# Kernel tuning notes

Measured on AMD Instinct MI355X. Metric: run time of the kernel, lower is better.

The kernel has to match this reference:

```python
import jax, jax.numpy as jnp
import numpy as np

N = 50000   # nodes
E = 800000  # directed edges (self-loops added inside reference)
F_IN, H, C = 128, 96, 32


def setup_inputs() -> dict:
    key = jax.random.key(0)
    ks = jax.random.split(key, 8)
    x = jax.random.normal(ks[0], (N, F_IN), dtype=jnp.float32)
    edge_index = jax.random.randint(ks[1], (2, E), 0, N, dtype=jnp.int64)
    W1 = jax.random.normal(ks[2], (F_IN, H), dtype=jnp.float32) * 0.05
    b1 = jnp.zeros((H,), dtype=jnp.float32)
    W2 = jax.random.normal(ks[3], (H, H), dtype=jnp.float32) * 0.05
    b2 = jnp.zeros((H,), dtype=jnp.float32)
    W3 = jax.random.normal(ks[4], (H, C), dtype=jnp.float32) * 0.05
    b3 = jnp.zeros((C,), dtype=jnp.float32)
    return {"x": x, "edge_index": edge_index, "W1": W1, "b1": b1,
            "W2": W2, "b2": b2, "W3": W3, "b3": b3}


def gcn_conv(x, W, b, src, dst, n):
    """PyG GCNConv: x' = D^{-1/2} (A+I) D^{-1/2} (x W) + b (self-loops in src/dst)."""
    xw = x @ W                                        # [n, out]
    ones = jnp.ones(src.shape[0], dtype=xw.dtype)
    deg = jax.ops.segment_sum(ones, dst, num_segments=n)
    dinv = jnp.where(deg > 0, jax.lax.rsqrt(jnp.maximum(deg, 1.0)), 0.0)
    norm = dinv[src] * dinv[dst]                      # [E+n]
    msg = norm[:, None] * xw[src]                     # gather + scale
    out = jax.ops.segment_sum(msg, dst, num_segments=n)  # scatter-add
    return out + b


def reference(x, edge_index, W1, b1, W2, b2, W3, b3):
    loop = jnp.arange(N, dtype=edge_index.dtype)
    src = jnp.concatenate([edge_index[0], loop])      # add self-loops once
    dst = jnp.concatenate([edge_index[1], loop])
    h = jax.nn.relu(gcn_conv(x, W1, b1, src, dst, N))   # dropout is identity (eval)
    h = jax.nn.relu(gcn_conv(h, W2, b2, src, dst, N))
    h = gcn_conv(h, W3, b3, src, dst, N)
    return jax.nn.log_softmax(h, axis=1)
```

## Files before the change

kernel.cpp:

```cpp
#include <hip/hip_runtime.h>
#include <hip/hip_fp16.h>


typedef _Float16 half8 __attribute__((ext_vector_type(8)));
typedef float f32x4 __attribute__((ext_vector_type(4)));

constexpr int CAP = 64;
constexpr int NPB = 128;
constexpr int NBINS_P = 512;
constexpr int EPB = 4096;
constexpr int BCAP = 2560;

__device__ inline unsigned char f_to_fp8(float f) {
    f = fminf(fmaxf(f, -448.0f), 448.0f);
    unsigned short u = __half_as_ushort(__float2half(f * 0.00390625f));
    unsigned short mag = (unsigned short)((u & 0x7FFF) + 0x40);
    return (unsigned char)(((u >> 8) & 0x80) | (mag >> 7));
}

__device__ inline float2 fp8x2_to_f2_scaled(unsigned int w) {
    unsigned int lo = ((w << 7) & 0x3F80u) | ((w << 8) & 0x8000u);
    unsigned int hi = ((w >> 1) & 0x3F80u) | (w & 0x8000u);
    union { unsigned int u; __half2 h; } cv;
    cv.u = lo | (hi << 16);
    return __half22float2(cv.h);
}

__global__ __launch_bounds__(256) void prep_kernel(const int* __restrict__ ei, int twoE,
                                                   int* __restrict__ flags,
                                                   int* __restrict__ bin_cnt,
                                                   const float* __restrict__ W1,
                                                   const float* __restrict__ W2,
                                                   const float* __restrict__ W3,
                                                   __half* __restrict__ Wt1,
                                                   __half* __restrict__ Wt2,
                                                   __half* __restrict__ Wt3) {
    if (blockIdx.x == 0) {
        if (threadIdx.x < 8) flags[threadIdx.x] = 0;
        for (int b = threadIdx.x; b < NBINS_P; b += 256) bin_cnt[b] = 0;
        __syncthreads();
        int c = 0;
        for (int j = threadIdx.x; j < 2048 && j < twoE; j += 256) {
            if ((j & 1) && ei[j] != 0) c++;
        }
        if (c) atomicAdd(&flags[4], c);
        return;
    }
    int i = (blockIdx.x - 1) * 256 + threadIdx.x;
    if (i < 128 * 96) {
        int f = i / 128, k = i - f * 128;
        Wt1[i] = __float2half(W1[(size_t)k * 96 + f]);
    } else if (i < 128 * 96 + 96 * 96) {
        int j = i - 128 * 96;
        int f = j / 96, k = j - f * 96;
        Wt2[j] = __float2half(W2[(size_t)k * 96 + f]);
    } else if (i < 128 * 96 + 96 * 96 + 96 * 32) {
        int j = i - 128 * 96 - 96 * 96;
        int f = j / 96, k = j - f * 96;
        Wt3[j] = __float2half(W3[(size_t)k * 32 + f]);
    }
}

__device__ inline int ld_idx(const int* ei, int half_, int i, int E, bool i64) {
    return i64 ? ei[2 * (half_ * (size_t)E + i)] : ei[half_ * (size_t)E + i];
}

__global__ __launch_bounds__(256) void part_kernel(const int* __restrict__ ei,
                                                   const int* __restrict__ flags,
                                                   int* __restrict__ bin_cnt,
                                                   int* __restrict__ bins, int E, int n) {
    __shared__ int hist[NBINS_P], excl[NBINS_P], cur[NBINS_P], gpos[NBINS_P];
    __shared__ int tmp[256];
    __shared__ int stage[EPB];
    const int tid = threadIdx.x;
    const bool i64 = (flags[4] == 0);
    for (int b = tid; b < NBINS_P; b += 256) hist[b] = 0;
    __syncthreads();

    int v[EPB / 256];
    const int base = blockIdx.x * EPB;
#pragma unroll
    for (int j = 0; j < EPB / 256; j++) {
        int i = base + j * 256 + tid;
        v[j] = -1;
        if (i < E) {
            int s = ld_idx(ei, 0, i, E, i64);
            int d = ld_idx(ei, 1, i, E, i64);
            if ((unsigned)s < (unsigned)n && (unsigned)d < (unsigned)n) {
                int bin = d >> 7, ln = d & 127;
                v[j] = (bin << 23) | (ln << 16) | s;
                atomicAdd(&hist[bin], 1);
            }
        }
    }
    __syncthreads();
    int a0 = hist[2 * tid], a1 = hist[2 * tid + 1];
    int pairsum = a0 + a1;
    tmp[tid] = pairsum;
    __syncthreads();
    for (int off = 1; off < 256; off <<= 1) {
        int t = (tid >= off) ? tmp[tid - off] : 0;
        __syncthreads();
        tmp[tid] += t;
        __syncthreads();
    }
    int S = tmp[tid] - pairsum;
    excl[2 * tid] = S;
    excl[2 * tid + 1] = S + a0;
    cur[2 * tid] = S;
    cur[2 * tid + 1] = S + a0;
    __syncthreads();
    for (int b = tid; b < NBINS_P; b += 256)
        gpos[b] = hist[b] ? atomicAdd(&bin_cnt[b], hist[b]) : 0;
#pragma unroll
    for (int j = 0; j < EPB / 256; j++) {
        if (v[j] != -1) {
            int bin = ((unsigned)v[j]) >> 23;
            int p = atomicAdd(&cur[bin], 1);
            stage[p] = v[j];
        }
    }
    __syncthreads();
    int total = excl[NBINS_P - 1] + hist[NBINS_P - 1];
    for (int i = tid; i < total; i += 256) {
        int w = stage[i];
        int bin = ((unsigned)w) >> 23;
        int k = gpos[bin] + (i - excl[bin]);
        if (k < BCAP) bins[(size_t)bin * BCAP + k] = w;
    }
}

__global__ __launch_bounds__(256) void build_kernel(const int* __restrict__ bin_cnt,
                                                    const int* __restrict__ bins,
                                                    int* __restrict__ cnt,
                                                    int* __restrict__ csr, int n) {
    __shared__ int lcsr[NPB * CAP];
    __shared__ int lcnt[NPB];
    const int b = blockIdx.x, tid = threadIdx.x;
    for (int i = tid; i < NPB; i += 256) lcnt[i] = 0;
    __syncthreads();
    int m = min(bin_cnt[b], BCAP);
    for (int i = tid; i < m; i += 256) {
        int w = bins[(size_t)b * BCAP + i];
        int ln = (w >> 16) & 127;
        int s = w & 0xFFFF;
        int p = atomicAdd(&lcnt[ln], 1);
        if (p < CAP) lcsr[ln * CAP + p] = s;
    }
    __syncthreads();
    const int node0 = b * NPB;
    for (int i = tid; i < NPB * CAP; i += 256) {
        int node = node0 + (i >> 6);
        if (node < n) csr[(size_t)node * CAP + (i & 63)] = lcsr[i];
    }
    for (int t = tid; t < NPB; t += 256)
        if (node0 + t < n) cnt[node0 + t] = lcnt[t];
}

__device__ inline half8 to_h8(float4 u0, float4 u1) {
    half8 r;
    r[0] = (_Float16)u0.x; r[1] = (_Float16)u0.y; r[2] = (_Float16)u0.z; r[3] = (_Float16)u0.w;
    r[4] = (_Float16)u1.x; r[5] = (_Float16)u1.y; r[6] = (_Float16)u1.z; r[7] = (_Float16)u1.w;
    return r;
}

template <int K, int F, bool XF32, bool OUT8>
__global__ __launch_bounds__(256) void gemm_mfma(const void* __restrict__ X,
                                                 const __half* __restrict__ Wt,
                                                 const int* __restrict__ cnt,
                                                 void* __restrict__ out, int n) {
    constexpr int KP = K + 8;
    constexpr int FT = F / 16;
    constexpr int KC = K / 32;
    __shared__ _Float16 Wl[F * KP];
    for (int i = threadIdx.x; i < F * (K / 8); i += 256) {
        int f = i / (K / 8), c = i - f * (K / 8);
        *(half8*)&Wl[f * KP + c * 8] = *(const half8*)&Wt[(size_t)f * K + c * 8];
    }
    __syncthreads();
    const int wave = threadIdx.x >> 6, lane = threadIdx.x & 63;
    const int node0 = (blockIdx.x * 4 + wave) * 16;
    if (node0 >= n) return;
    const int m = lane & 15, q = lane >> 4;
    const int arow = min(node0 + m, n - 1);

    half8 af[KC];
    if (XF32) {
        const float* xp = (const float*)X + (size_t)arow * K + q * 8;
#pragma unroll
        for (int kc = 0; kc < KC; kc++) {
            float4 u0 = *(const float4*)(xp + kc * 32);
            float4 u1 = *(const float4*)(xp + kc * 32 + 4);
            af[kc] = to_h8(u0, u1);
        }
    } else {
        const __half* xp = (const __half*)X + (size_t)arow * K + q * 8;
#pragma unroll
        for (int kc = 0; kc < KC; kc++) af[kc] = *(const half8*)(xp + kc * 32);
    }

    f32x4 acc[FT];
#pragma unroll
    for (int t = 0; t < FT; t++) acc[t] = (f32x4)0.f;
#pragma unroll
    for (int kc = 0; kc < KC; kc++) {
#pragma unroll
        for (int t = 0; t < FT; t++) {
            half8 b = *(const half8*)&Wl[(t * 16 + m) * KP + kc * 32 + q * 8];
            acc[t] = __builtin_amdgcn_mfma_f32_16x16x32_f16(af[kc], b, acc[t], 0, 0, 0);
        }
    }
    float dv[4];
#pragma unroll
    for (int r = 0; r < 4; r++) {
        int node = node0 + q * 4 + r;
        dv[r] = (node < n) ? rsqrtf(1.0f + (float)cnt[node]) : 0.f;
    }
#pragma unroll
    for (int t = 0; t < FT; t++)
#pragma unroll
        for (int r = 0; r < 4; r++) {
            int node = node0 + q * 4 + r;
            if (node < n) {
                float vv = acc[t][r] * dv[r];
                if (OUT8)
                    ((unsigned char*)out)[(size_t)node * F + t * 16 + m] = f_to_fp8(vv);
                else
                    ((__half*)out)[(size_t)node * F + t * 16 + m] = __float2half(vv);
            }
        }
}

__global__ __launch_bounds__(256) void agg96_fp8(const unsigned char* __restrict__ xws,
                                                 const int* __restrict__ cnt,
                                                 const int* __restrict__ csr,
                                                 const float* __restrict__ bias,
                                                 __half2* __restrict__ out, int n) {
    int node = blockIdx.x * 4 + (threadIdx.x >> 6);
    int lane = threadIdx.x & 63;
    if (node >= n) return;
    const bool act = lane < 48;
    int deg = cnt[node];
    float dvs = rsqrtf(1.0f + (float)deg) * 256.0f;
    float2 a = {0.f, 0.f};
    if (act) {
        unsigned int w = ((const unsigned short*)(xws + (size_t)node * 96))[lane];
        a = fp8x2_to_f2_scaled(w);
    }
    int e = node * CAP, e1 = e + min(deg, CAP);
    for (; e + 7 < e1; e += 8) {
        int u[8];
#pragma unroll
        for (int j = 0; j < 8; j++) u[j] = csr[e + j];
        if (act) {
            unsigned int w[8];
#pragma unroll
            for (int j = 0; j < 8; j++)
                w[j] = ((const unsigned short*)(xws + (size_t)u[j] * 96))[lane];
#pragma unroll
            for (int j = 0; j < 8; j++) {
                float2 f = fp8x2_to_f2_scaled(w[j]);
                a.x += f.x; a.y += f.y;
            }
        }
    }
    for (; e < e1; e++) {
        int u = csr[e];
        if (act) {
            unsigned int w = ((const unsigned short*)(xws + (size_t)u * 96))[lane];
            float2 f = fp8x2_to_f2_scaled(w);
            a.x += f.x; a.y += f.y;
        }
    }
    if (act) {
        float2 b = *(const float2*)&bias[lane * 2];
        float rx = fmaxf(fmaf(dvs, a.x, b.x), 0.f);
        float ry = fmaxf(fmaf(dvs, a.y, b.y), 0.f);
        out[(size_t)node * 48 + lane] = __floats2half2_rn(rx, ry);
    }
}

__global__ __launch_bounds__(256) void agg32_lsm(const __half2* __restrict__ xws,
                                                 const int* __restrict__ cnt,
                                                 const int* __restrict__ csr,
                                                 const float* __restrict__ bias,
                                                 float* __restrict__ out, int n) {
    int node = blockIdx.x * 4 + (threadIdx.x >> 6);
    int lane = threadIdx.x & 63;
    if (node >= n) return;
    const bool act = lane < 16;
    int deg = cnt[node];
    float dv = rsqrtf(1.0f + (float)deg);
    float2 a = {0.f, 0.f};
    if (act) a = __half22float2(xws[(size_t)node * 16 + lane]);
    int e = node * CAP, e1 = e + min(deg, CAP);
    for (; e + 7 < e1; e += 8) {
        int u[8];
#pragma unroll
        for (int j = 0; j < 8; j++) u[j] = csr[e + j];
        if (act) {
#pragma unroll
            for (int j = 0; j < 8; j++) {
                float2 f = __half22float2(xws[(size_t)u[j] * 16 + lane]);
                a.x += f.x; a.y += f.y;
            }
        }
    }
    for (; e < e1; e++) {
        int u = csr[e];
        if (act) {
            float2 f = __half22float2(xws[(size_t)u * 16 + lane]);
            a.x += f.x; a.y += f.y;
        }
    }
    if (act) {
        float2 b = *(const float2*)&bias[lane * 2];
        float rx = fmaf(dv, a.x, b.x), ry = fmaf(dv, a.y, b.y);
        float mx = fmaxf(rx, ry);
        mx = fmaxf(mx, __shfl_xor(mx, 1));
        mx = fmaxf(mx, __shfl_xor(mx, 2));
        mx = fmaxf(mx, __shfl_xor(mx, 4));
        mx = fmaxf(mx, __shfl_xor(mx, 8));
        float s = expf(rx - mx) + expf(ry - mx);
        s += __shfl_xor(s, 1);
        s += __shfl_xor(s, 2);
        s += __shfl_xor(s, 4);
        s += __shfl_xor(s, 8);
        float ls = logf(s);
        ((float2*)out)[(size_t)node * 16 + lane] = {rx - mx - ls, ry - mx - ls};
    }
}

extern "C" void kernel_launch(void* const* d_in, const int* in_sizes, int n_in,
                              void* d_out, int out_size, void* d_ws, size_t ws_size,
                              hipStream_t stream) {
    const float* x  = (const float*)d_in[0];
    const int*   ei = (const int*)d_in[1];
    const float* W1 = (const float*)d_in[2];
    const float* b1 = (const float*)d_in[3];
    const float* W2 = (const float*)d_in[4];
    const float* b2 = (const float*)d_in[5];
    const float* W3 = (const float*)d_in[6];
    const float* b3 = (const float*)d_in[7];
    float* out = (float*)d_out;

    const int N_ = in_sizes[0] / 128;
    const int E_ = in_sizes[1] / 2;
    const int NBINS = (N_ + NPB - 1) / NPB;

    char* base = (char*)d_ws;
    size_t off = 0;
    auto take = [&](size_t bytes) {
        void* p = base + off;
        off = (off + bytes + 255) & ~(size_t)255;
        return p;
    };
    int*    flags   = (int*)take(4 * 8);
    int*    bin_cnt = (int*)take(4 * NBINS_P);
    int*    bins    = (int*)take(4 * (size_t)NBINS * BCAP);
    int*    cnt     = (int*)take(4 * (size_t)N_);
    int*    csr     = (int*)take(4 * (size_t)N_ * CAP);
    __half* Wt1     = (__half*)take(2 * 128 * 96);
    __half* Wt2     = (__half*)take(2 * 96 * 96);
    __half* Wt3     = (__half*)take(2 * 96 * 32);
    unsigned char* bufA = (unsigned char*)take(2 * (size_t)N_ * 96);
    __half* bufB    = (__half*)take(2 * (size_t)N_ * 96);

    const int prepBlocks = 1 + (128 * 96 + 96 * 96 + 96 * 32 + 255) / 256;
    prep_kernel<<<prepBlocks, 256, 0, stream>>>(ei, in_sizes[1], flags, bin_cnt,
                                                W1, W2, W3, Wt1, Wt2, Wt3);
    part_kernel<<<(E_ + EPB - 1) / EPB, 256, 0, stream>>>(ei, flags, bin_cnt, bins, E_, N_);
    build_kernel<<<NBINS, 256, 0, stream>>>(bin_cnt, bins, cnt, csr, N_);

    const int gGemm = (N_ + 63) / 64;
    const int gAgg  = (N_ + 3) / 4;

    gemm_mfma<128, 96, true, true><<<gGemm, 256, 0, stream>>>(x, Wt1, cnt, bufA, N_);
    agg96_fp8<<<gAgg, 256, 0, stream>>>(bufA, cnt, csr, b1, (__half2*)bufB, N_);
    gemm_mfma<96, 96, false, true><<<gGemm, 256, 0, stream>>>(bufB, Wt2, cnt, bufA, N_);
    agg96_fp8<<<gAgg, 256, 0, stream>>>(bufA, cnt, csr, b2, (__half2*)bufB, N_);
    gemm_mfma<96, 32, false, false><<<gGemm, 256, 0, stream>>>(bufB, Wt3, cnt, bufA, N_);
    agg32_lsm<<<gAgg, 256, 0, stream>>>((const __half2*)bufA, cnt, csr, b3, out, N_);
}
```

Before: 245.9 us.

## Compress CSR to 16-bit indices and split neighbor gathers across lane groups

Neighbor indices are stored as 16-bit shorts instead of 32-bit ints. This halves CSR memory traffic in the build and in all three aggregations, and index rows are now read with wide vector loads. The 96-wide aggregation has two 24-lane groups each gather 4 fp8 bytes from alternating neighbors and then combine through a shuffle. The 32-wide aggregation uses four 16-lane groups to process four neighbors in parallel with a shuffle reduction. The short indices only work because node IDs fit in 16 bits (N=50000), which the existing bin encoding already assumed.

```diff
diff --git a/kernel.cpp b/kernel.cpp
--- a/kernel.cpp
+++ b/kernel.cpp
@@ -24,6 +24,12 @@
     union { unsigned int u; __half2 h; } cv;
     cv.u = lo | (hi << 16);
     return __half22float2(cv.h);
+}
+
+__device__ inline float4 fp8x4_to_f4_scaled(unsigned int w) {
+    float2 lo = fp8x2_to_f2_scaled(w & 0xFFFFu);
+    float2 hi = fp8x2_to_f2_scaled(w >> 16);
+    return {lo.x, lo.y, hi.x, hi.y};
 }
 
 __global__ __launch_bounds__(256) void prep_kernel(const int* __restrict__ ei, int twoE,
@@ -133,8 +139,8 @@
 __global__ __launch_bounds__(256) void build_kernel(const int* __restrict__ bin_cnt,
                                                     const int* __restrict__ bins,
                                                     int* __restrict__ cnt,
-                                                    int* __restrict__ csr, int n) {
-    __shared__ int lcsr[NPB * CAP];
+                                                    unsigned short* __restrict__ csr, int n) {
+    __shared__ unsigned short lcsr[NPB * CAP];
     __shared__ int lcnt[NPB];
     const int b = blockIdx.x, tid = threadIdx.x;
     for (int i = tid; i < NPB; i += 256) lcnt[i] = 0;
@@ -143,15 +149,16 @@
     for (int i = tid; i < m; i += 256) {
         int w = bins[(size_t)b * BCAP + i];
         int ln = (w >> 16) & 127;
-        int s = w & 0xFFFF;
         int p = atomicAdd(&lcnt[ln], 1);
-        if (p < CAP) lcsr[ln * CAP + p] = s;
+        if (p < CAP) lcsr[ln * CAP + p] = (unsigned short)(w & 0xFFFF);
     }
     __syncthreads();
     const int node0 = b * NPB;
-    for (int i = tid; i < NPB * CAP; i += 256) {
-        int node = node0 + (i >> 6);
-        if (node < n) csr[(size_t)node * CAP + (i & 63)] = lcsr[i];
+    const unsigned int* l32 = (const unsigned int*)lcsr;
+    unsigned int* c32 = (unsigned int*)(csr + (size_t)node0 * CAP);
+    for (int i = tid; i < NPB * CAP / 2; i += 256) {
+        int node = node0 + (i >> 5);
+        if (node < n) c32[i] = l32[i];
     }
     for (int t = tid; t < NPB; t += 256)
         if (node0 + t < n) cnt[node0 + t] = lcnt[t];
@@ -233,88 +240,111 @@
 
 __global__ __launch_bounds__(256) void agg96_fp8(const unsigned char* __restrict__ xws,
                                                  const int* __restrict__ cnt,
-                                                 const int* __restrict__ csr,
+                                                 const unsigned short* __restrict__ csr,
                                                  const float* __restrict__ bias,
-                                                 __half2* __restrict__ out, int n) {
+                                                 __half* __restrict__ out, int n) {
     int node = blockIdx.x * 4 + (threadIdx.x >> 6);
     int lane = threadIdx.x & 63;
     if (node >= n) return;
+    const int g = lane < 24 ? 0 : 1;
+    const int c = g ? lane - 24 : lane;
     const bool act = lane < 48;
     int deg = cnt[node];
+    int m = min(deg, CAP);
     float dvs = rsqrtf(1.0f + (float)deg) * 256.0f;
-    float2 a = {0.f, 0.f};
-    if (act) {
-        unsigned int w = ((const unsigned short*)(xws + (size_t)node * 96))[lane];
-        a = fp8x2_to_f2_scaled(w);
-    }
-    int e = node * CAP, e1 = e + min(deg, CAP);
-    for (; e + 7 < e1; e += 8) {
-        int u[8];
-#pragma unroll
-        for (int j = 0; j < 8; j++) u[j] = csr[e + j];
+    const unsigned short* row = csr + (size_t)node * CAP;
+    float4 a = {0.f, 0.f, 0.f, 0.f};
+    if (lane < 24) {
+        unsigned int w = *(const unsigned int*)(xws + (size_t)node * 96 + c * 4);
+        a = fp8x4_to_f4_scaled(w);
+    }
+    int e = 0;
+    for (; e + 8 <= m; e += 8) {
+        uint4 pr = *(const uint4*)&row[e];
         if (act) {
-            unsigned int w[8];
-#pragma unroll
-            for (int j = 0; j < 8; j++)
-                w[j] = ((const unsigned short*)(xws + (size_t)u[j] * 96))[lane];
-#pragma unroll
-            for (int j = 0; j < 8; j++) {
-                float2 f = fp8x2_to_f2_scaled(w[j]);
-                a.x += f.x; a.y += f.y;
+            unsigned int w[4];
+            int u0 = g ? (pr.x >> 16) : (pr.x & 0xFFFF);
+            int u1 = g ? (pr.y >> 16) : (pr.y & 0xFFFF);
+            int u2 = g ? (pr.z >> 16) : (pr.z & 0xFFFF);
+            int u3 = g ? (pr.w >> 16) : (pr.w & 0xFFFF);
+            w[0] = *(const unsigned int*)(xws + (size_t)u0 * 96 + c * 4);
+            w[1] = *(const unsigned int*)(xws + (size_t)u1 * 96 + c * 4);
+            w[2] = *(const unsigned int*)(xws + (size_t)u2 * 96 + c * 4);
+            w[3] = *(const unsigned int*)(xws + (size_t)u3 * 96 + c * 4);
+#pragma unroll
+            for (int j = 0; j < 4; j++) {
+                float4 f = fp8x4_to_f4_scaled(w[j]);
+                a.x += f.x; a.y += f.y; a.z += f.z; a.w += f.w;
             }
         }
     }
-    for (; e < e1; e++) {
-        int u = csr[e];
+    for (; e + 2 <= m; e += 2) {
+        unsigned int pr = *(const unsigned int*)&row[e];
         if (act) {
-            unsigned int w = ((const unsigned short*)(xws + (size_t)u * 96))[lane];
-            float2 f = fp8x2_to_f2_scaled(w);
-            a.x += f.x; a.y += f.y;
-        }
-    }
-    if (act) {
-        float2 b = *(const float2*)&bias[lane * 2];
-        float rx = fmaxf(fmaf(dvs, a.x, b.x), 0.f);
-        float ry = fmaxf(fmaf(dvs, a.y, b.y), 0.f);
-        out[(size_t)node * 48 + lane] = __floats2half2_rn(rx, ry);
-    }
-}
-
-__global__ __launch_bounds__(256) void agg32_lsm(const __half2* __restrict__ xws,
+            int u = g ? (pr >> 16) : (pr & 0xFFFF);
+            unsigned int w = *(const unsigned int*)(xws + (size_t)u * 96 + c * 4);
+            float4 f = fp8x4_to_f4_scaled(w);
+            a.x += f.x; a.y += f.y; a.z += f.z; a.w += f.w;
+        }
+    }
+    if (e < m && lane < 24) {
+        int u = row[e];
+        unsigned int w = *(const unsigned int*)(xws + (size_t)u * 96 + c * 4);
+        float4 f = fp8x4_to_f4_scaled(w);
+        a.x += f.x; a.y += f.y; a.z += f.z; a.w += f.w;
+    }
+    float px = __shfl(a.x, lane + 24);
+    float py = __shfl(a.y, lane + 24);
+    float pz = __shfl(a.z, lane + 24);
+    float pw = __shfl(a.w, lane + 24);
+    if (lane < 24) {
+        a.x += px; a.y += py; a.z += pz; a.w += pw;
+        float4 bb = *(const float4*)&bias[c * 4];
+        float r0 = fmaxf(fmaf(dvs, a.x, bb.x), 0.f);
+        float r1 = fmaxf(fmaf(dvs, a.y, bb.y), 0.f);
+        float r2 = fmaxf(fmaf(dvs, a.z, bb.z), 0.f);
+        float r3 = fmaxf(fmaf(dvs, a.w, bb.w), 0.f);
+        union { __half2 h[2]; uint2 u; } pk;
+        pk.h[0] = __floats2half2_rn(r0, r1);
+        pk.h[1] = __floats2half2_rn(r2, r3);
+        *(uint2*)(out + (size_t)node * 96 + c * 4) = pk.u;
+    }
+}
+
+__global__ __launch_bounds__(256) void agg32_lsm(const __half* __restrict__ xws,
                                                  const int* __restrict__ cnt,
-                                                 const int* __restrict__ csr,
+                                                 const unsigned short* __restrict__ csr,
                                                  const float* __restrict__ bias,
                                                  float* __restrict__ out, int n) {
     int node = blockIdx.x * 4 + (threadIdx.x >> 6);
     int lane = threadIdx.x & 63;
     if (node >= n) return;
-    const bool act = lane < 16;
+    const int g = lane >> 4, l = lane & 15;
     int deg = cnt[node];
+    int m = min(deg, CAP);
     float dv = rsqrtf(1.0f + (float)deg);
+    const unsigned short* row = csr + (size_t)node * CAP;
     float2 a = {0.f, 0.f};
-    if (act) a = __half22float2(xws[(size_t)node * 16 + lane]);
-    int e = node * CAP, e1 = e + min(deg, CAP);
-    for (; e + 7 < e1; e += 8) {
-        int u[8];
-#pragma unroll
-        for (int j = 0; j < 8; j++) u[j] = csr[e + j];
-        if (act) {
-#pragma unroll
-            for (int j = 0; j < 8; j++) {
-                float2 f = __half22float2(xws[(size_t)u[j] * 16 + lane]);
-                a.x += f.x; a.y += f.y;
-            }
-        }
-    }
-    for (; e < e1; e++) {
-        int u = csr[e];
-        if (act) {
-            float2 f = __half22float2(xws[(size_t)u * 16 + lane]);
+    if (g == 0) a = __half22float2(*(const __half2*)(xws + (size_t)node * 32 + l * 2));
+    int e = 0;
+    for (; e + 4 <= m; e += 4) {
+        uint2 pr = *(const uint2*)&row[e];
+        unsigned int h = (g & 2) ? pr.y : pr.x;
+        int u = (g & 1) ? (int)(h >> 16) : (int)(h & 0xFFFF);
+        float2 f = __half22float2(*(const __half2*)(xws + (size_t)u * 32 + l * 2));
+        a.x += f.x; a.y += f.y;
+    }
+    for (; e < m; e++) {
+        if (g == 0) {
+            int u = row[e];
+            float2 f = __half22float2(*(const __half2*)(xws + (size_t)u * 32 + l * 2));
             a.x += f.x; a.y += f.y;
         }
     }
-    if (act) {
-        float2 b = *(const float2*)&bias[lane * 2];
+    a.x += __shfl_xor(a.x, 16); a.y += __shfl_xor(a.y, 16);
+    a.x += __shfl_xor(a.x, 32); a.y += __shfl_xor(a.y, 32);
+    if (g == 0) {
+        float2 b = *(const float2*)&bias[l * 2];
         float rx = fmaf(dv, a.x, b.x), ry = fmaf(dv, a.y, b.y);
         float mx = fmaxf(rx, ry);
         mx = fmaxf(mx, __shfl_xor(mx, 1));
@@ -327,7 +357,7 @@
         s += __shfl_xor(s, 4);
         s += __shfl_xor(s, 8);
         float ls = logf(s);
-        ((float2*)out)[(size_t)node * 16 + lane] = {rx - mx - ls, ry - mx - ls};
+        ((float2*)out)[(size_t)node * 16 + l] = {rx - mx - ls, ry - mx - ls};
     }
 }
 
@@ -359,7 +389,7 @@
     int*    bin_cnt = (int*)take(4 * NBINS_P);
     int*    bins    = (int*)take(4 * (size_t)NBINS * BCAP);
     int*    cnt     = (int*)take(4 * (size_t)N_);
-    int*    csr     = (int*)take(4 * (size_t)N_ * CAP);
+    unsigned short* csr = (unsigned short*)take(2 * (size_t)N_ * CAP);
     __half* Wt1     = (__half*)take(2 * 128 * 96);
     __half* Wt2     = (__half*)take(2 * 96 * 96);
     __half* Wt3     = (__half*)take(2 * 96 * 32);
@@ -376,9 +406,9 @@
     const int gAgg  = (N_ + 3) / 4;
 
     gemm_mfma<128, 96, true, true><<<gGemm, 256, 0, stream>>>(x, Wt1, cnt, bufA, N_);
-    agg96_fp8<<<gAgg, 256, 0, stream>>>(bufA, cnt, csr, b1, (__half2*)bufB, N_);
+    agg96_fp8<<<gAgg, 256, 0, stream>>>(bufA, cnt, csr, b1, bufB, N_);
     gemm_mfma<96, 96, false, true><<<gGemm, 256, 0, stream>>>(bufB, Wt2, cnt, bufA, N_);
-    agg96_fp8<<<gAgg, 256, 0, stream>>>(bufA, cnt, csr, b2, (__half2*)bufB, N_);
+    agg96_fp8<<<gAgg, 256, 0, stream>>>(bufA, cnt, csr, b2, bufB, N_);
     gemm_mfma<96, 32, false, false><<<gGemm, 256, 0, stream>>>(bufB, Wt3, cnt, bufA, N_);
-    agg32_lsm<<<gAgg, 256, 0, stream>>>((const __half2*)bufA, cnt, csr, b3, out, N_);
-}
+    agg32_lsm<<<gAgg, 256, 0, stream>>>((const __half*)bufA, cnt, csr, b3, out, N_);
+}
```

After: 234.3 us. -4.7%, faster.
